# Kernel tuning notes

Hardware: AMD Instinct MI355X
Metric: run time of the kernel (lower is better)

The kernel has to match this reference:

```python
import jax, jax.numpy as jnp
import numpy as np

ALPHA = 0.2   # LeakyReLU negative slope
T_STEPS = 10  # diffusion iterations


def setup_inputs() -> dict:
    key = jax.random.key(0)
    ks = jax.random.split(key, 7)
    N, F, H, C, E, NTRAIN = 8192, 512, 64, 10, 262144, 512
    # glorot-ish scales so exp(leaky_relu(.)) stays in range
    h = jax.random.normal(ks[0], (N, F), jnp.float32)
    W = jax.random.normal(ks[1], (H, F), jnp.float32) * 0.059
    a = jax.random.normal(ks[2], (2 * H, 1), jnp.float32) * 0.12
    W1 = jax.random.normal(ks[3], (C, F), jnp.float32) * 0.06
    features = jax.random.normal(ks[4], (N, F), jnp.float32)
    edge_index = jax.random.randint(ks[5], (2, E), 0, N, dtype=jnp.int32)
    idx_train = jnp.arange(NTRAIN, dtype=jnp.int32)
    labels = jax.random.randint(ks[6], (N,), 0, C, dtype=jnp.int32)
    return {"h": h, "W": W, "a": a, "W1": W1, "features": features,
            "edge_index": edge_index, "idx_train": idx_train, "labels": labels}


def reference(h, W, a, W1, features, edge_index, idx_train, labels):
    N = h.shape[0]
    C = W1.shape[0]
    # ---- CalAttenA ----
    Wh = h @ W.T                                   # [N, H]
    src, dst = edge_index[0], edge_index[1]
    f12 = jnp.concatenate([Wh[src], Wh[dst]], axis=1)   # [E, 2H]
    e = jnp.exp(jax.nn.leaky_relu(f12 @ a, negative_slope=ALPHA)).ravel()  # [E]
    A = jnp.zeros((N, N), Wh.dtype).at[src, dst].set(e)
    s1 = A.sum(axis=1)
    diag = jnp.arange(N)
    A = A.at[diag, diag].add(jnp.where(s1 == 0, 1.0, 0.0).astype(Wh.dtype))
    A = A / A.sum(axis=1, keepdims=True)           # row-normalized attention
    # ---- PoiConv ----
    Kg = jnp.zeros((C, N), Wh.dtype).at[labels[idx_train], idx_train].set(1.0)
    c = Kg.sum(axis=1) / idx_train.shape[0]        # [C]
    b = Kg.T.at[idx_train].add(-c)                 # [N, C] (idx_train unique)
    # D = diag(1 / rowsum(A + 1e-10*I)); eye only touches the diagonal so
    # rowsum is rowsum(A) + 1e-10 == 1 + 1e-10 after normalization.
    d = 1.0 / (A.sum(axis=1) + 1e-10)              # [N]
    P = d[:, None] * A.T                           # D @ A^T
    Db = d[:, None] * b                            # D @ b
    ut = jnp.zeros((N, C), Wh.dtype)
    for t in range(1, T_STEPS + 1):
        ut = P @ ut + Db
        if t == T_STEPS - 3:  # isadj == False branch; dropout inactive (eval)
            ut = ut + features @ W1.T
    return ut
```

## Files before the change

### kernel.cpp

```cpp
#include <hip/hip_runtime.h>
#include <stdint.h>

#define NN 8192
#define FF 512
#define HH 64
#define CC 10
#define EE 262144
#define NTR 512
#define ALPHA_NS 0.2f

#define CAP 96u
#define EMPTY 0xFFFFFFFFu
#define ROWS_PB 32

__device__ __forceinline__ float dot4(float4 a, float4 b){
    return a.x*b.x + a.y*b.y + a.z*b.z + a.w*b.w;
}

__global__ __launch_bounds__(1024) void k_init(
    const float* __restrict__ W, const float* __restrict__ a,
    const float* __restrict__ h, const float* __restrict__ feat,
    const float* __restrict__ W1, const int* __restrict__ idx_tr,
    const int* __restrict__ labels,
    uint32_t* __restrict__ csrc2, float* __restrict__ s1,
    float* __restrict__ s_src, float* __restrict__ s_dst,
    float* __restrict__ FW, float* __restrict__ Db)
{
    __shared__ float v0l[FF];
    __shared__ float v1l[FF];
    __shared__ int chist[CC];
    __shared__ float cvecl[CC];
    __shared__ uint8_t lmark[ROWS_PB];

    const int tid = threadIdx.x;
    const int b   = blockIdx.x;
    const int rbase = b * ROWS_PB;

    const uint32_t spb = (NN * CAP) / 256u;
    for (uint32_t i = tid; i < spb; i += 1024) csrc2[(uint32_t)b*spb + i] = EMPTY;
    if (tid < ROWS_PB) s1[rbase + tid] = 0.f;

    {
        int f = tid & (FF-1);
        const float* av = (tid < FF) ? a : (a + HH);
        float acc = 0.f;
        for (int hh = 0; hh < HH; ++hh) acc += W[hh*FF + f] * av[hh];
        if (tid < FF) v0l[f] = acc; else v1l[f] = acc;
    }

    if (tid < ROWS_PB) lmark[tid] = 0;
    if (tid < CC) chist[tid] = 0;
    __syncthreads();
    if (tid < NTR){
        int node = idx_tr[tid];
        atomicAdd(&chist[labels[node]], 1);
        unsigned lr = (unsigned)(node - rbase);
        if (lr < (unsigned)ROWS_PB) lmark[lr] = 1;
    }
    __syncthreads();
    if (tid < CC) cvecl[tid] = (float)chist[tid] / (float)NTR;
    __syncthreads();

    {
        const int wid = tid >> 6, lane = tid & 63;
        const float4* v0 = (const float4*)v0l;
        const float4* v1 = (const float4*)v1l;
        #pragma unroll
        for (int rr = 0; rr < 2; ++rr){
            int row = rbase + wid*2 + rr;
            const float4* hr = (const float4*)(h + (size_t)row*FF);
            float4 x0 = hr[lane*2], x1 = hr[lane*2+1];
            float a0 = dot4(x0, v0[lane*2]) + dot4(x1, v0[lane*2+1]);
            float a1 = dot4(x0, v1[lane*2]) + dot4(x1, v1[lane*2+1]);
            #pragma unroll
            for (int off = 32; off >= 1; off >>= 1){
                a0 += __shfl_xor(a0, off);
                a1 += __shfl_xor(a1, off);
            }
            if (lane == 0){ s_src[row] = a0; s_dst[row] = a1; }

            const float4* fr = (const float4*)(feat + (size_t)row*FF);
            float4 f0 = fr[lane*2], f1 = fr[lane*2+1];
            float acc[CC];
            #pragma unroll
            for (int c = 0; c < CC; ++c){
                const float4* wr = (const float4*)(W1 + c*FF);
                acc[c] = dot4(f0, wr[lane*2]) + dot4(f1, wr[lane*2+1]);
            }
            #pragma unroll
            for (int c = 0; c < CC; ++c){
                float r = acc[c];
                #pragma unroll
                for (int off = 32; off >= 1; off >>= 1) r += __shfl_xor(r, off);
                acc[c] = r;
            }
            if (lane == 0){
                #pragma unroll
                for (int c = 0; c < CC; ++c) FW[row*CC + c] = acc[c];
            }
        }
    }

    if (tid < ROWS_PB*CC){
        int il = tid / CC, c = tid - il*CC;
        int row = rbase + il;
        float v = 0.f;
        if (lmark[il]) v = ((labels[row] == c) ? 1.0f : 0.0f) - cvecl[c];
        Db[row*CC + c] = v;
    }
}

__global__ void k_build(const int* __restrict__ ei, const float* __restrict__ s_src,
                        const float* __restrict__ s_dst,
                        uint32_t* __restrict__ csrc2, float* __restrict__ e2,
                        float* __restrict__ s1)
{
    int k = blockIdx.x*256 + threadIdx.x;
    int src = ei[k], dst = ei[EE + k];
    uint32_t base = (uint32_t)dst * CAP;
    uint32_t p = (uint32_t)(((uint64_t)((uint32_t)src * 2654435761u) * CAP) >> 32);
    float z = s_src[src] + s_dst[dst];
    z = (z >= 0.f) ? z : ALPHA_NS * z;
    float e = expf(z);
    for (uint32_t it = 0; it < CAP; ++it){
        uint32_t prev = atomicCAS(&csrc2[base + p], EMPTY, (uint32_t)src);
        if (prev == EMPTY){
            e2[base + p] = e;
            atomicAdd(&s1[src], e);
            break;
        }
        if (prev == (uint32_t)src) break;
        p = (p + 1u == CAP) ? 0u : p + 1u;
    }
}

__global__ __launch_bounds__(1024) void k_fixup(
    uint32_t* __restrict__ csrc2, float* __restrict__ e2,
    float* __restrict__ s1, uint32_t* __restrict__ cnt,
    const float* __restrict__ Db, float* __restrict__ uhA)
{
    const int tid = threadIdx.x;
    const int wid = tid >> 6, lane = tid & 63;
    const int row = blockIdx.x*16 + wid;
    const uint32_t base = (uint32_t)row * CAP;

    uint32_t c0 = csrc2[base + lane];
    uint32_t c1 = (lane < (int)(CAP - 64u)) ? csrc2[base + 64 + lane] : EMPTY;
    float    e0 = e2[base + lane];
    float    e1 = (lane < (int)(CAP - 64u)) ? e2[base + 64 + lane] : 0.f;

    uint64_t m0 = __ballot(c0 != EMPTY);
    uint64_t m1 = __ballot((lane < (int)(CAP - 64u)) && c1 != EMPTY);
    uint64_t below = (lane == 63) ? ~0ull >> 1 : ((1ull << lane) - 1ull);
    below = ((1ull << lane) - 1ull);
    uint32_t t0   = (uint32_t)__popcll(m0);
    uint32_t pos0 = (uint32_t)__popcll(m0 & below);
    uint32_t pos1 = t0 + (uint32_t)__popcll(m1 & below);
    uint32_t total = t0 + (uint32_t)__popcll(m1);

    __syncthreads();

    if (c0 != EMPTY){ csrc2[base + pos0] = c0; e2[base + pos0] = e0; }
    if (lane < (int)(CAP - 64u) && c1 != EMPTY){ csrc2[base + pos1] = c1; e2[base + pos1] = e1; }

    float s1v = 0.f;
    if (lane == 0){
        s1v = s1[row];
        if (s1v == 0.f){
            csrc2[base + total] = (uint32_t)row;
            e2[base + total] = 1.0f;
            total += 1u;
            s1[row] = 1.0f;
            s1v = 1.0f;
        }
        cnt[row] = total;
    }
    s1v = __shfl(s1v, 0);
    if (lane < CC) uhA[row*CC + lane] = Db[row*CC + lane] / s1v;
}

__global__ __launch_bounds__(1024) void k_spmv(
    const uint32_t* __restrict__ cnt, const uint32_t* __restrict__ csrc2,
    const float* __restrict__ e2, const float* __restrict__ uh_in,
    const float* __restrict__ Db, const float* __restrict__ FW,
    const float* __restrict__ s1, float* __restrict__ uout,
    int add_fw, int final_step)
{
    const int tid = threadIdx.x;
    const int wid = tid >> 6, lane = tid & 63;
    const int sub = lane >> 5, l32 = lane & 31;
    const int row = (blockIdx.x*16 + wid)*2 + sub;
    const uint32_t base = (uint32_t)row * CAP;
    const uint32_t n = cnt[row];

    float acc[CC];
    #pragma unroll
    for (int c = 0; c < CC; ++c) acc[c] = 0.f;
    for (uint32_t p = (uint32_t)l32; p < n; p += 32u){
        uint32_t sr = csrc2[base + p];
        float w = e2[base + p];
        const float2* u2 = (const float2*)(uh_in + (size_t)sr*CC);
        #pragma unroll
        for (int q = 0; q < 5; ++q){
            float2 v = u2[q];
            acc[2*q]   += w * v.x;
            acc[2*q+1] += w * v.y;
        }
    }
    #pragma unroll
    for (int c = 0; c < CC; ++c){
        float r = acc[c];
        #pragma unroll
        for (int off = 16; off >= 1; off >>= 1) r += __shfl_xor(r, off);
        acc[c] = r;
    }
    if (l32 == 0){
        const float* db = Db + row*CC;
        float* o = uout + row*CC;
        float t[CC];
        #pragma unroll
        for (int c = 0; c < CC; ++c) t[c] = acc[c] + db[c];
        if (add_fw){
            const float* fw = FW + row*CC;
            #pragma unroll
            for (int c = 0; c < CC; ++c) t[c] += fw[c];
        }
        if (final_step){
            #pragma unroll
            for (int c = 0; c < CC; ++c) o[c] = t[c];
        } else {
            float inv = 1.0f / s1[row];
            #pragma unroll
            for (int c = 0; c < CC; ++c) o[c] = t[c] * inv;
        }
    }
}

extern "C" void kernel_launch(void* const* d_in, const int* in_sizes, int n_in,
                              void* d_out, int out_size, void* d_ws, size_t ws_size,
                              hipStream_t stream){
    const float* h    = (const float*)d_in[0];
    const float* W    = (const float*)d_in[1];
    const float* a    = (const float*)d_in[2];
    const float* W1   = (const float*)d_in[3];
    const float* feat = (const float*)d_in[4];
    const int* ei     = (const int*)d_in[5];
    const int* idx_tr = (const int*)d_in[6];
    const int* labels = (const int*)d_in[7];
    float* out = (float*)d_out;

    char* wsp = (char*)d_ws;
    auto alloc = [&](size_t bytes)->void*{
        void* p = (void*)wsp;
        wsp += (bytes + 255) & ~(size_t)255;
        return p;
    };
    uint32_t* csrc2 = (uint32_t*)alloc((size_t)NN*CAP*4);
    float*    e2    = (float*)   alloc((size_t)NN*CAP*4);
    float*    s1    = (float*)   alloc(NN*4);
    uint32_t* cnt   = (uint32_t*)alloc(NN*4);
    float*    s_src = (float*)   alloc(NN*4);
    float*    s_dst = (float*)   alloc(NN*4);
    float*    FW    = (float*)   alloc((size_t)NN*CC*4);
    float*    Db    = (float*)   alloc((size_t)NN*CC*4);
    float*    uhA   = (float*)   alloc((size_t)NN*CC*4);
    float*    uhB   = (float*)   alloc((size_t)NN*CC*4);

    k_init <<<256, 1024, 0, stream>>>(W, a, h, feat, W1, idx_tr, labels,
                                      csrc2, s1, s_src, s_dst, FW, Db);
    k_build<<<EE/256, 256, 0, stream>>>(ei, s_src, s_dst, csrc2, e2, s1);
    k_fixup<<<NN/16, 1024, 0, stream>>>(csrc2, e2, s1, cnt, Db, uhA);

    float* cur = uhA;
    float* nxt = uhB;
    for (int t = 2; t <= 10; ++t){
        float* dst = (t == 10) ? out : nxt;
        k_spmv<<<NN/32, 1024, 0, stream>>>(cnt, csrc2, e2, cur, Db, FW, s1, dst,
                                           (t == 7) ? 1 : 0, (t == 10) ? 1 : 0);
        float* tmp = cur; cur = dst; nxt = tmp;
    }
}
```

Measured before the change: 110.4 us.

## Interleave hash table into uint2 slots and prenormalize edge weights by source row sum

Source index and edge weight now share one 8-byte slot instead of sitting in two separate arrays, so each SpMV edge read is a single 64-bit load. The fixup kernel divides each weight by the source node's row sum ahead of time. This removes the per-row scale in every SpMV step and the separate uhA init, since the iteration now starts directly from Db. The build loop also reads a slot before attempting the CAS, to skip atomics on occupied slots, and the ping-pong buffer logic is rewritten, which is somewhat convoluted.

```diff
diff --git a/kernel.cpp b/kernel.cpp
--- a/kernel.cpp
+++ b/kernel.cpp
@@ -12,6 +12,7 @@
 #define CAP 96u
 #define EMPTY 0xFFFFFFFFu
 #define ROWS_PB 32
+#define SLOTS_PB ((NN*CAP)/256u)
 
 __device__ __forceinline__ float dot4(float4 a, float4 b){
     return a.x*b.x + a.y*b.y + a.z*b.z + a.w*b.w;
@@ -22,7 +23,7 @@
     const float* __restrict__ h, const float* __restrict__ feat,
     const float* __restrict__ W1, const int* __restrict__ idx_tr,
     const int* __restrict__ labels,
-    uint32_t* __restrict__ csrc2, float* __restrict__ s1,
+    uint2* __restrict__ tab, float* __restrict__ s1,
     float* __restrict__ s_src, float* __restrict__ s_dst,
     float* __restrict__ FW, float* __restrict__ Db)
 {
@@ -36,8 +37,8 @@
     const int b   = blockIdx.x;
     const int rbase = b * ROWS_PB;
 
-    const uint32_t spb = (NN * CAP) / 256u;
-    for (uint32_t i = tid; i < spb; i += 1024) csrc2[(uint32_t)b*spb + i] = EMPTY;
+    for (uint32_t i = tid; i < SLOTS_PB; i += 1024)
+        tab[(uint32_t)b*SLOTS_PB + i] = make_uint2(EMPTY, 0u);
     if (tid < ROWS_PB) s1[rbase + tid] = 0.f;
 
     {
@@ -112,8 +113,7 @@
 
 __global__ void k_build(const int* __restrict__ ei, const float* __restrict__ s_src,
                         const float* __restrict__ s_dst,
-                        uint32_t* __restrict__ csrc2, float* __restrict__ e2,
-                        float* __restrict__ s1)
+                        uint2* __restrict__ tab, float* __restrict__ s1)
 {
     int k = blockIdx.x*256 + threadIdx.x;
     int src = ei[k], dst = ei[EE + k];
@@ -123,88 +123,83 @@
     z = (z >= 0.f) ? z : ALPHA_NS * z;
     float e = expf(z);
     for (uint32_t it = 0; it < CAP; ++it){
-        uint32_t prev = atomicCAS(&csrc2[base + p], EMPTY, (uint32_t)src);
-        if (prev == EMPTY){
-            e2[base + p] = e;
-            atomicAdd(&s1[src], e);
-            break;
-        }
-        if (prev == (uint32_t)src) break;
+        uint32_t cur = tab[base + p].x;
+        if (cur == (uint32_t)src) break;
+        if (cur == EMPTY){
+            uint32_t prev = atomicCAS(&tab[base + p].x, EMPTY, (uint32_t)src);
+            if (prev == EMPTY){
+                tab[base + p].y = __float_as_uint(e);
+                atomicAdd(&s1[src], e);
+                break;
+            }
+            if (prev == (uint32_t)src) break;
+        }
         p = (p + 1u == CAP) ? 0u : p + 1u;
     }
 }
 
 __global__ __launch_bounds__(1024) void k_fixup(
-    uint32_t* __restrict__ csrc2, float* __restrict__ e2,
-    float* __restrict__ s1, uint32_t* __restrict__ cnt,
-    const float* __restrict__ Db, float* __restrict__ uhA)
+    uint2* __restrict__ tab, const float* __restrict__ s1,
+    uint32_t* __restrict__ cnt)
 {
     const int tid = threadIdx.x;
     const int wid = tid >> 6, lane = tid & 63;
     const int row = blockIdx.x*16 + wid;
     const uint32_t base = (uint32_t)row * CAP;
 
-    uint32_t c0 = csrc2[base + lane];
-    uint32_t c1 = (lane < (int)(CAP - 64u)) ? csrc2[base + 64 + lane] : EMPTY;
-    float    e0 = e2[base + lane];
-    float    e1 = (lane < (int)(CAP - 64u)) ? e2[base + 64 + lane] : 0.f;
-
-    uint64_t m0 = __ballot(c0 != EMPTY);
-    uint64_t m1 = __ballot((lane < (int)(CAP - 64u)) && c1 != EMPTY);
-    uint64_t below = (lane == 63) ? ~0ull >> 1 : ((1ull << lane) - 1ull);
-    below = ((1ull << lane) - 1ull);
+    uint2 v0 = tab[base + lane];
+    uint2 v1 = (lane < (int)(CAP - 64u)) ? tab[base + 64 + lane] : make_uint2(EMPTY, 0u);
+
+    uint64_t m0 = __ballot(v0.x != EMPTY);
+    uint64_t m1 = __ballot((lane < (int)(CAP - 64u)) && v1.x != EMPTY);
+    uint64_t below = (1ull << lane) - 1ull;
     uint32_t t0   = (uint32_t)__popcll(m0);
     uint32_t pos0 = (uint32_t)__popcll(m0 & below);
     uint32_t pos1 = t0 + (uint32_t)__popcll(m1 & below);
     uint32_t total = t0 + (uint32_t)__popcll(m1);
 
-    __syncthreads();
-
-    if (c0 != EMPTY){ csrc2[base + pos0] = c0; e2[base + pos0] = e0; }
-    if (lane < (int)(CAP - 64u) && c1 != EMPTY){ csrc2[base + pos1] = c1; e2[base + pos1] = e1; }
-
-    float s1v = 0.f;
+    if (v0.x != EMPTY){
+        float w = __uint_as_float(v0.y) / s1[v0.x];
+        tab[base + pos0] = make_uint2(v0.x, __float_as_uint(w));
+    }
+    if (lane < (int)(CAP - 64u) && v1.x != EMPTY){
+        float w = __uint_as_float(v1.y) / s1[v1.x];
+        tab[base + pos1] = make_uint2(v1.x, __float_as_uint(w));
+    }
+
     if (lane == 0){
-        s1v = s1[row];
-        if (s1v == 0.f){
-            csrc2[base + total] = (uint32_t)row;
-            e2[base + total] = 1.0f;
+        if (s1[row] == 0.f){
+            tab[base + total] = make_uint2((uint32_t)row, __float_as_uint(1.0f));
             total += 1u;
-            s1[row] = 1.0f;
-            s1v = 1.0f;
         }
         cnt[row] = total;
     }
-    s1v = __shfl(s1v, 0);
-    if (lane < CC) uhA[row*CC + lane] = Db[row*CC + lane] / s1v;
 }
 
 __global__ __launch_bounds__(1024) void k_spmv(
-    const uint32_t* __restrict__ cnt, const uint32_t* __restrict__ csrc2,
-    const float* __restrict__ e2, const float* __restrict__ uh_in,
-    const float* __restrict__ Db, const float* __restrict__ FW,
-    const float* __restrict__ s1, float* __restrict__ uout,
-    int add_fw, int final_step)
+    const uint32_t* __restrict__ cnt, const uint2* __restrict__ tab,
+    const float* __restrict__ uh_in, const float* __restrict__ Db,
+    const float* __restrict__ FW, float* __restrict__ uout, int add_fw)
 {
     const int tid = threadIdx.x;
     const int wid = tid >> 6, lane = tid & 63;
     const int sub = lane >> 5, l32 = lane & 31;
     const int row = (blockIdx.x*16 + wid)*2 + sub;
-    const uint32_t base = (uint32_t)row * CAP;
+    const uint2* tp = tab + (uint32_t)row * CAP;
     const uint32_t n = cnt[row];
 
     float acc[CC];
     #pragma unroll
     for (int c = 0; c < CC; ++c) acc[c] = 0.f;
     for (uint32_t p = (uint32_t)l32; p < n; p += 32u){
-        uint32_t sr = csrc2[base + p];
-        float w = e2[base + p];
-        const float2* u2 = (const float2*)(uh_in + (size_t)sr*CC);
+        uint2 v = tp[p];
+        float w = __uint_as_float(v.y);
+        const float2* u2 = (const float2*)(uh_in + (size_t)v.x*CC);
         #pragma unroll
         for (int q = 0; q < 5; ++q){
-            float2 v = u2[q];
-            acc[2*q]   += w * v.x;
-            acc[2*q+1] += w * v.y;
+            float2 u = u2[q];
+            acc[2*q]   += w * u.x;
+            acc[2*q+1] += w * u.y;
         }
     }
     #pragma unroll
@@ -217,21 +212,13 @@
     if (l32 == 0){
         const float* db = Db + row*CC;
         float* o = uout + row*CC;
-        float t[CC];
-        #pragma unroll
-        for (int c = 0; c < CC; ++c) t[c] = acc[c] + db[c];
         if (add_fw){
             const float* fw = FW + row*CC;
             #pragma unroll
-            for (int c = 0; c < CC; ++c) t[c] += fw[c];
-        }
-        if (final_step){
-            #pragma unroll
-            for (int c = 0; c < CC; ++c) o[c] = t[c];
+            for (int c = 0; c < CC; ++c) o[c] = acc[c] + db[c] + fw[c];
         } else {
-            float inv = 1.0f / s1[row];
-            #pragma unroll
-            for (int c = 0; c < CC; ++c) o[c] = t[c] * inv;
+            #pragma unroll
+            for (int c = 0; c < CC; ++c) o[c] = acc[c] + db[c];
         }
     }
 }
@@ -255,28 +242,32 @@
         wsp += (bytes + 255) & ~(size_t)255;
         return p;
     };
-    uint32_t* csrc2 = (uint32_t*)alloc((size_t)NN*CAP*4);
-    float*    e2    = (float*)   alloc((size_t)NN*CAP*4);
+    uint2*    tab   = (uint2*)   alloc((size_t)NN*CAP*8);
     float*    s1    = (float*)   alloc(NN*4);
     uint32_t* cnt   = (uint32_t*)alloc(NN*4);
     float*    s_src = (float*)   alloc(NN*4);
     float*    s_dst = (float*)   alloc(NN*4);
     float*    FW    = (float*)   alloc((size_t)NN*CC*4);
     float*    Db    = (float*)   alloc((size_t)NN*CC*4);
-    float*    uhA   = (float*)   alloc((size_t)NN*CC*4);
-    float*    uhB   = (float*)   alloc((size_t)NN*CC*4);
+    float*    uA    = (float*)   alloc((size_t)NN*CC*4);
+    float*    uB    = (float*)   alloc((size_t)NN*CC*4);
 
     k_init <<<256, 1024, 0, stream>>>(W, a, h, feat, W1, idx_tr, labels,
-                                      csrc2, s1, s_src, s_dst, FW, Db);
-    k_build<<<EE/256, 256, 0, stream>>>(ei, s_src, s_dst, csrc2, e2, s1);
-    k_fixup<<<NN/16, 1024, 0, stream>>>(csrc2, e2, s1, cnt, Db, uhA);
-
-    float* cur = uhA;
-    float* nxt = uhB;
+                                      tab, s1, s_src, s_dst, FW, Db);
+    k_build<<<EE/256, 256, 0, stream>>>(ei, s_src, s_dst, tab, s1);
+    k_fixup<<<NN/16, 1024, 0, stream>>>(tab, s1, cnt);
+
+    const float* cur = Db;
+    float* nxt = uB;
+    float* alt = uA;
     for (int t = 2; t <= 10; ++t){
         float* dst = (t == 10) ? out : nxt;
-        k_spmv<<<NN/32, 1024, 0, stream>>>(cnt, csrc2, e2, cur, Db, FW, s1, dst,
-                                           (t == 7) ? 1 : 0, (t == 10) ? 1 : 0);
-        float* tmp = cur; cur = dst; nxt = tmp;
-    }
-}
+        k_spmv<<<NN/32, 1024, 0, stream>>>(cnt, tab, cur, Db, FW, dst,
+                                           (t == 7) ? 1 : 0);
+        cur = dst;
+        nxt = alt;
+        alt = dst == out ? alt : dst;
+        if (t == 2){ nxt = uA; alt = uB; }
+        else { float* tmp; tmp = (cur == uA) ? uB : uA; nxt = tmp; alt = (float*)cur; }
+    }
+}
```

After: 125.4 us. 1.14x slower.

## Fold row normalization into edge weights and pad state to 12 floats for vector loads

Applied to the files above, without the earlier changes.

The per-step division by s1 on the destination row is replaced by pre-dividing each edge weight by the source row's s1 during fixup. The weight and index go into an interleaved uint2 table, so each spmv step needs one 8-byte load per edge. The state vectors are padded to 12 floats so gathers use three float4 loads, and 16 lanes now handle each row. This adds a second compacted edge table in memory, and the first step now reads Db directly.

```diff
diff --git a/kernel.cpp b/kernel.cpp
--- a/kernel.cpp
+++ b/kernel.cpp
@@ -5,6 +5,7 @@
 #define FF 512
 #define HH 64
 #define CC 10
+#define PAD 12
 #define EE 262144
 #define NTR 512
 #define ALPHA_NS 0.2f
@@ -12,6 +13,7 @@
 #define CAP 96u
 #define EMPTY 0xFFFFFFFFu
 #define ROWS_PB 32
+#define SLOTS_PB ((NN*CAP)/256u)
 
 __device__ __forceinline__ float dot4(float4 a, float4 b){
     return a.x*b.x + a.y*b.y + a.z*b.z + a.w*b.w;
@@ -36,8 +38,8 @@
     const int b   = blockIdx.x;
     const int rbase = b * ROWS_PB;
 
-    const uint32_t spb = (NN * CAP) / 256u;
-    for (uint32_t i = tid; i < spb; i += 1024) csrc2[(uint32_t)b*spb + i] = EMPTY;
+    for (uint32_t i = tid; i < SLOTS_PB; i += 1024)
+        csrc2[(uint32_t)b*SLOTS_PB + i] = EMPTY;
     if (tid < ROWS_PB) s1[rbase + tid] = 0.f;
 
     {
@@ -96,17 +98,17 @@
             }
             if (lane == 0){
                 #pragma unroll
-                for (int c = 0; c < CC; ++c) FW[row*CC + c] = acc[c];
+                for (int c = 0; c < CC; ++c) FW[row*PAD + c] = acc[c];
             }
         }
     }
 
-    if (tid < ROWS_PB*CC){
-        int il = tid / CC, c = tid - il*CC;
+    if (tid < ROWS_PB*PAD){
+        int il = tid / PAD, c = tid - il*PAD;
         int row = rbase + il;
         float v = 0.f;
-        if (lmark[il]) v = ((labels[row] == c) ? 1.0f : 0.0f) - cvecl[c];
-        Db[row*CC + c] = v;
+        if (c < CC && lmark[il]) v = ((labels[row] == c) ? 1.0f : 0.0f) - cvecl[c];
+        Db[row*PAD + c] = v;
     }
 }
 
@@ -135,9 +137,9 @@
 }
 
 __global__ __launch_bounds__(1024) void k_fixup(
-    uint32_t* __restrict__ csrc2, float* __restrict__ e2,
-    float* __restrict__ s1, uint32_t* __restrict__ cnt,
-    const float* __restrict__ Db, float* __restrict__ uhA)
+    const uint32_t* __restrict__ csrc2, const float* __restrict__ e2,
+    const float* __restrict__ s1, uint2* __restrict__ tabc,
+    uint32_t* __restrict__ cnt)
 {
     const int tid = threadIdx.x;
     const int wid = tid >> 6, lane = tid & 63;
@@ -151,88 +153,75 @@
 
     uint64_t m0 = __ballot(c0 != EMPTY);
     uint64_t m1 = __ballot((lane < (int)(CAP - 64u)) && c1 != EMPTY);
-    uint64_t below = (lane == 63) ? ~0ull >> 1 : ((1ull << lane) - 1ull);
-    below = ((1ull << lane) - 1ull);
+    uint64_t below = (1ull << lane) - 1ull;
     uint32_t t0   = (uint32_t)__popcll(m0);
     uint32_t pos0 = (uint32_t)__popcll(m0 & below);
     uint32_t pos1 = t0 + (uint32_t)__popcll(m1 & below);
     uint32_t total = t0 + (uint32_t)__popcll(m1);
 
-    __syncthreads();
-
-    if (c0 != EMPTY){ csrc2[base + pos0] = c0; e2[base + pos0] = e0; }
-    if (lane < (int)(CAP - 64u) && c1 != EMPTY){ csrc2[base + pos1] = c1; e2[base + pos1] = e1; }
-
-    float s1v = 0.f;
+    if (c0 != EMPTY){
+        float w = e0 / s1[c0];
+        tabc[base + pos0] = make_uint2(c0, __float_as_uint(w));
+    }
+    if (lane < (int)(CAP - 64u) && c1 != EMPTY){
+        float w = e1 / s1[c1];
+        tabc[base + pos1] = make_uint2(c1, __float_as_uint(w));
+    }
+
     if (lane == 0){
-        s1v = s1[row];
-        if (s1v == 0.f){
-            csrc2[base + total] = (uint32_t)row;
-            e2[base + total] = 1.0f;
+        if (s1[row] == 0.f){
+            tabc[base + total] = make_uint2((uint32_t)row, __float_as_uint(1.0f));
             total += 1u;
-            s1[row] = 1.0f;
-            s1v = 1.0f;
         }
         cnt[row] = total;
     }
-    s1v = __shfl(s1v, 0);
-    if (lane < CC) uhA[row*CC + lane] = Db[row*CC + lane] / s1v;
-}
-
-__global__ __launch_bounds__(1024) void k_spmv(
-    const uint32_t* __restrict__ cnt, const uint32_t* __restrict__ csrc2,
-    const float* __restrict__ e2, const float* __restrict__ uh_in,
-    const float* __restrict__ Db, const float* __restrict__ FW,
-    const float* __restrict__ s1, float* __restrict__ uout,
+}
+
+__global__ __launch_bounds__(256) void k_spmv(
+    const uint32_t* __restrict__ cnt, const uint2* __restrict__ tabc,
+    const float* __restrict__ uh_in, const float* __restrict__ Db,
+    const float* __restrict__ FW, float* __restrict__ uout,
     int add_fw, int final_step)
 {
     const int tid = threadIdx.x;
     const int wid = tid >> 6, lane = tid & 63;
-    const int sub = lane >> 5, l32 = lane & 31;
-    const int row = (blockIdx.x*16 + wid)*2 + sub;
-    const uint32_t base = (uint32_t)row * CAP;
+    const int l16 = lane & 15;
+    const int row = blockIdx.x*16 + wid*4 + (lane >> 4);
+    const uint2* tp = tabc + (uint32_t)row * CAP;
     const uint32_t n = cnt[row];
 
-    float acc[CC];
+    float acc[PAD];
     #pragma unroll
-    for (int c = 0; c < CC; ++c) acc[c] = 0.f;
-    for (uint32_t p = (uint32_t)l32; p < n; p += 32u){
-        uint32_t sr = csrc2[base + p];
-        float w = e2[base + p];
-        const float2* u2 = (const float2*)(uh_in + (size_t)sr*CC);
-        #pragma unroll
-        for (int q = 0; q < 5; ++q){
-            float2 v = u2[q];
-            acc[2*q]   += w * v.x;
-            acc[2*q+1] += w * v.y;
-        }
+    for (int c = 0; c < PAD; ++c) acc[c] = 0.f;
+    for (uint32_t p = (uint32_t)l16; p < n; p += 16u){
+        uint2 v = tp[p];
+        float w = __uint_as_float(v.y);
+        const float4* u4 = (const float4*)(uh_in + (size_t)v.x*PAD);
+        float4 u0 = u4[0], u1 = u4[1], u2 = u4[2];
+        acc[0] += w*u0.x; acc[1] += w*u0.y; acc[2]  += w*u0.z; acc[3]  += w*u0.w;
+        acc[4] += w*u1.x; acc[5] += w*u1.y; acc[6]  += w*u1.z; acc[7]  += w*u1.w;
+        acc[8] += w*u2.x; acc[9] += w*u2.y; acc[10] += w*u2.z; acc[11] += w*u2.w;
     }
     #pragma unroll
-    for (int c = 0; c < CC; ++c){
+    for (int c = 0; c < PAD; ++c){
         float r = acc[c];
         #pragma unroll
-        for (int off = 16; off >= 1; off >>= 1) r += __shfl_xor(r, off);
+        for (int off = 8; off >= 1; off >>= 1) r += __shfl_xor(r, off, 16);
         acc[c] = r;
     }
-    if (l32 == 0){
-        const float* db = Db + row*CC;
-        float* o = uout + row*CC;
-        float t[CC];
-        #pragma unroll
-        for (int c = 0; c < CC; ++c) t[c] = acc[c] + db[c];
-        if (add_fw){
-            const float* fw = FW + row*CC;
-            #pragma unroll
-            for (int c = 0; c < CC; ++c) t[c] += fw[c];
-        }
-        if (final_step){
-            #pragma unroll
-            for (int c = 0; c < CC; ++c) o[c] = t[c];
-        } else {
-            float inv = 1.0f / s1[row];
-            #pragma unroll
-            for (int c = 0; c < CC; ++c) o[c] = t[c] * inv;
-        }
+    float v = acc[0];
+    #pragma unroll
+    for (int c = 1; c < PAD; ++c) v = (l16 == c) ? acc[c] : v;
+    if (l16 < CC){
+        v += Db[row*PAD + l16];
+        if (add_fw) v += FW[row*PAD + l16];
+    } else {
+        v = 0.f;
+    }
+    if (final_step){
+        if (l16 < CC) uout[(size_t)row*CC + l16] = v;
+    } else {
+        if (l16 < PAD) uout[(size_t)row*PAD + l16] = v;
     }
 }
 
@@ -257,26 +246,26 @@
     };
     uint32_t* csrc2 = (uint32_t*)alloc((size_t)NN*CAP*4);
     float*    e2    = (float*)   alloc((size_t)NN*CAP*4);
+    uint2*    tabc  = (uint2*)   alloc((size_t)NN*CAP*8);
     float*    s1    = (float*)   alloc(NN*4);
     uint32_t* cnt   = (uint32_t*)alloc(NN*4);
     float*    s_src = (float*)   alloc(NN*4);
     float*    s_dst = (float*)   alloc(NN*4);
-    float*    FW    = (float*)   alloc((size_t)NN*CC*4);
-    float*    Db    = (float*)   alloc((size_t)NN*CC*4);
-    float*    uhA   = (float*)   alloc((size_t)NN*CC*4);
-    float*    uhB   = (float*)   alloc((size_t)NN*CC*4);
+    float*    FW    = (float*)   alloc((size_t)NN*PAD*4);
+    float*    Db    = (float*)   alloc((size_t)NN*PAD*4);
+    float*    uA    = (float*)   alloc((size_t)NN*PAD*4);
+    float*    uB    = (float*)   alloc((size_t)NN*PAD*4);
 
     k_init <<<256, 1024, 0, stream>>>(W, a, h, feat, W1, idx_tr, labels,
                                       csrc2, s1, s_src, s_dst, FW, Db);
     k_build<<<EE/256, 256, 0, stream>>>(ei, s_src, s_dst, csrc2, e2, s1);
-    k_fixup<<<NN/16, 1024, 0, stream>>>(csrc2, e2, s1, cnt, Db, uhA);
-
-    float* cur = uhA;
-    float* nxt = uhB;
+    k_fixup<<<NN/16, 1024, 0, stream>>>(csrc2, e2, s1, tabc, cnt);
+
+    const float* cur = Db;
     for (int t = 2; t <= 10; ++t){
-        float* dst = (t == 10) ? out : nxt;
-        k_spmv<<<NN/32, 1024, 0, stream>>>(cnt, csrc2, e2, cur, Db, FW, s1, dst,
-                                           (t == 7) ? 1 : 0, (t == 10) ? 1 : 0);
-        float* tmp = cur; cur = dst; nxt = tmp;
-    }
-}
+        float* dst = (t == 10) ? out : ((t & 1) ? uB : uA);
+        k_spmv<<<NN/16, 256, 0, stream>>>(cnt, tabc, cur, Db, FW, dst,
+                                          (t == 7) ? 1 : 0, (t == 10) ? 1 : 0);
+        cur = dst;
+    }
+}
```

Result: faster. 103.0 us (-6.7%).
